# Kernel optimization log

Measured on AMD Instinct MI355X. Metric: run time of the kernel, lower is better.

## Reference

```python
import jax, jax.numpy as jnp
import numpy as np

N_SVC, N_NODE, N_POD = 50000, 20000, 100000
F = 128          # svc/instance/node feature dims (all 128 per init_kwargs)
HID = 128        # hidden_size
OUT = 64         # out_channel
E_SVC, E_PN, E_NP = 1600000, 100000, 100000


def _graph_conv(x, src, dst, n_src, n_dst, W, b):
    """DGL GraphConv with norm='both': D_dst^{-1/2} A D_src^{-1/2} X W + b."""
    ones = jnp.ones(src.shape[0], dtype=x.dtype)
    deg_src = jnp.clip(jax.ops.segment_sum(ones, src, num_segments=n_src), 1.0)
    deg_dst = jnp.clip(jax.ops.segment_sum(ones, dst, num_segments=n_dst), 1.0)
    # normalize at source, gather, scatter-sum to dst, normalize at dst
    h = x * jax.lax.rsqrt(deg_src)[:, None]          # [n_src, F]
    msg = h[src]                                      # [E, F] gather (memory-bound)
    agg = jax.ops.segment_sum(msg, dst, num_segments=n_dst)  # [n_dst, F]
    agg = agg * jax.lax.rsqrt(deg_dst)[:, None]
    return agg @ W + b                                # [n_dst, HID]


def _leaky(h):
    return jnp.where(h > 0, h, 0.01 * h)


def setup_inputs() -> dict:
    key = jax.random.key(0)
    ks = jax.random.split(key, 16)
    d = {
        "x_svc": jax.random.normal(ks[0], (N_SVC, F), jnp.float32),
        "x_pod": jax.random.normal(ks[1], (N_POD, F), jnp.float32),
        "x_node": jax.random.normal(ks[2], (N_NODE, F), jnp.float32),
        "svc_src": jax.random.randint(ks[3], (E_SVC,), 0, N_SVC, jnp.int32),
        "svc_dst": jax.random.randint(ks[4], (E_SVC,), 0, N_SVC, jnp.int32),
        "pod_node_src": jax.random.randint(ks[5], (E_PN,), 0, N_POD, jnp.int32),
        "pod_node_dst": jax.random.randint(ks[6], (E_PN,), 0, N_NODE, jnp.int32),
        "node_pod_src": jax.random.randint(ks[7], (E_NP,), 0, N_NODE, jnp.int32),
        "node_pod_dst": jax.random.randint(ks[8], (E_NP,), 0, N_POD, jnp.int32),
        # GraphConv weights per edge type
        "W_call": jax.random.normal(ks[9], (F, HID), jnp.float32) * (1.0 / np.sqrt(F)),
        "b_call": jnp.zeros((HID,), jnp.float32),
        "W_in": jax.random.normal(ks[10], (F, HID), jnp.float32) * (1.0 / np.sqrt(F)),
        "b_in": jnp.zeros((HID,), jnp.float32),
        "W_ni": jax.random.normal(ks[11], (F, HID), jnp.float32) * (1.0 / np.sqrt(F)),
        "b_ni": jnp.zeros((HID,), jnp.float32),
        # per-node-type output Linear (hidden -> out_channel)
        "W_lin_svc": jax.random.normal(ks[12], (HID, OUT), jnp.float32) * (1.0 / np.sqrt(HID)),
        "b_lin_svc": jnp.zeros((OUT,), jnp.float32),
        "W_lin_node": jax.random.normal(ks[13], (HID, OUT), jnp.float32) * (1.0 / np.sqrt(HID)),
        "b_lin_node": jnp.zeros((OUT,), jnp.float32),
        "W_lin_pod": jax.random.normal(ks[14], (HID, OUT), jnp.float32) * (1.0 / np.sqrt(HID)),
        "b_lin_pod": jnp.zeros((OUT,), jnp.float32),
    }
    return d


def reference(x_svc, x_pod, x_node,
              svc_src, svc_dst, pod_node_src, pod_node_dst,
              node_pod_src, node_pod_dst,
              W_call, b_call, W_in, b_in, W_ni, b_ni,
              W_lin_svc, b_lin_svc, W_lin_node, b_lin_node,
              W_lin_pod, b_lin_pod):
    # HeteroGraphConv (sum aggregate; each dst type receives one edge type here)
    h_svc = _graph_conv(x_svc, svc_src, svc_dst, N_SVC, N_SVC, W_call, b_call)
    h_node = _graph_conv(x_pod, pod_node_src, pod_node_dst, N_POD, N_NODE, W_in, b_in)
    h_pod = _graph_conv(x_node, node_pod_src, node_pod_dst, N_NODE, N_POD, W_ni, b_ni)
    # per-node-type LeakyReLU + Linear
    o_svc = _leaky(h_svc) @ W_lin_svc + b_lin_svc    # [N_SVC, OUT]
    o_node = _leaky(h_node) @ W_lin_node + b_lin_node  # [N_NODE, OUT]
    o_pod = _leaky(h_pod) @ W_lin_pod + b_lin_pod    # [N_POD, OUT]
    return jnp.concatenate([o_svc, o_node, o_pod], axis=0)  # [N_SVC+N_NODE+N_POD, OUT]
```

## Files before the change

kernel.cpp:

```cpp
#include <hip/hip_runtime.h>

typedef __attribute__((ext_vector_type(8))) short short8;
typedef __attribute__((ext_vector_type(4))) float floatx4;

#define N_SVC  50000
#define N_NODE 20000
#define N_POD  100000
#define E_SVC  1600000
#define E_PN   100000
#define E_NP   100000
#define N_TOT  170000
#define E_TOT  1800000
#define NBUCK  1329
#define NBLK   256
#define PER_BLK 7032
#define P_SVC_BASE  0
#define P_NODE_BASE 50048
#define P_POD_BASE  70080
#define P_TOT       170112
#define SVC_WAVES   50048
#define SVC_BLOCKS  12512
#define NP_WAVES    30016
#define NP_BLOCKS   7504

__device__ __forceinline__ unsigned short f2bf(float f) {
  union { float f; unsigned u; } v; v.f = f;
  unsigned r = v.u + 0x7FFFu + ((v.u >> 16) & 1u);
  return (unsigned short)(r >> 16);
}
__device__ __forceinline__ unsigned pack_bf2(float a, float b) {
  return (unsigned)f2bf(a) | ((unsigned)f2bf(b) << 16);
}
__device__ __forceinline__ float bfl(unsigned u) { union { unsigned u; float f; } v; v.u = u << 16; return v.f; }
__device__ __forceinline__ float bfh(unsigned u) { union { unsigned u; float f; } v; v.u = u & 0xFFFF0000u; return v.f; }

__device__ __forceinline__ int dbase_of(int b) {
  if (b <= 391) return b * 6144;
  if (b <= 547) return 2402304 + (b - 391) * 1536;
  return 2641920 + (b - 547) * 512;
}
#define DST_CAP_TOT 3042304
__device__ __forceinline__ int sbase_of(int b) {
  if (b <= 391) return b * 6144;
  if (b <= 1171) return 2402304 + (b - 391) * 512;
  return 2801664 + (b - 1171) * 1536;
}
#define SRC_CAP_TOT 3044352

__device__ __forceinline__ void load_edge(int i,
    const int* __restrict__ svcS, const int* __restrict__ svcD,
    const int* __restrict__ pnS, const int* __restrict__ pnD,
    const int* __restrict__ npS, const int* __restrict__ npD,
    int& S, int& D) {
  if (i < E_SVC)             { S = svcS[i];                         D = svcD[i]; }
  else if (i < E_SVC + E_PN) { int j = i - E_SVC;        S = pnS[j] + 50000;  D = pnD[j] + 50000; }
  else                       { int j = i - E_SVC - E_PN; S = npS[j] + 150000; D = npD[j] + 70000; }
}

__global__ void wprep_init(const float* __restrict__ W0, const float* __restrict__ W1,
                           const float* __restrict__ W2, const float* __restrict__ L0,
                           const float* __restrict__ L1, const float* __restrict__ L2,
                           unsigned short* __restrict__ Wt, unsigned short* __restrict__ Wt2,
                           int* __restrict__ dcur, int* __restrict__ scur) {
  int i = blockIdx.x * 256 + threadIdx.x;
  if (i < NBUCK) { dcur[i] = dbase_of(i); scur[i] = sbase_of(i); }
  if (i < 3 * 16384) {
    int t = i / 16384, r = i % 16384, n = r / 128, k = r % 128;
    const float* W = (t == 0) ? W0 : ((t == 1) ? W1 : W2);
    Wt[i] = f2bf(W[k * 128 + n]);
  } else if (i < 3 * 16384 + 3 * 8192) {
    int j = i - 3 * 16384;
    int t = j / 8192, r = j % 8192, n = r / 128, k = r % 128;
    const float* L = (t == 0) ? L0 : ((t == 1) ? L1 : L2);
    Wt2[j] = f2bf(L[k * 64 + n]);
  }
}

__global__ __launch_bounds__(1024) void scatter_onepass(
    const int* __restrict__ svcS, const int* __restrict__ svcD,
    const int* __restrict__ pnS, const int* __restrict__ pnD,
    const int* __restrict__ npS, const int* __restrict__ npD,
    int* __restrict__ dcur, int* __restrict__ scur,
    unsigned* __restrict__ dstbuf, unsigned char* __restrict__ srcbuf) {
  __shared__ int ldc[NBUCK], lsc[NBUCK];
  const int tid = threadIdx.x;
  for (int t = tid; t < NBUCK; t += 1024) { ldc[t] = 0; lsc[t] = 0; }
  __syncthreads();
  const int lo = blockIdx.x * PER_BLK;
  const int hi = (lo + PER_BLK < E_TOT) ? lo + PER_BLK : E_TOT;
  int Sv[7], Dv[7];
  #pragma unroll
  for (int k = 0; k < 7; ++k) {
    int e = lo + tid + k * 1024;
    if (e < hi) {
      load_edge(e, svcS, svcD, pnS, pnD, npS, npD, Sv[k], Dv[k]);
      atomicAdd(&ldc[Dv[k] >> 7], 1);
      atomicAdd(&lsc[Sv[k] >> 7], 1);
    } else Sv[k] = -1;
  }
  __syncthreads();
  for (int t = tid; t < NBUCK; t += 1024) {
    int c = ldc[t];  ldc[t] = c ? atomicAdd(&dcur[t], c) : 0;
    int c2 = lsc[t]; lsc[t] = c2 ? atomicAdd(&scur[t], c2) : 0;
  }
  __syncthreads();
  #pragma unroll
  for (int k = 0; k < 7; ++k) {
    if (Sv[k] >= 0) {
      int p = atomicAdd(&ldc[Dv[k] >> 7], 1);
      dstbuf[p] = ((unsigned)(Dv[k] & 127) << 18) | (unsigned)Sv[k];
      int q = atomicAdd(&lsc[Sv[k] >> 7], 1);
      srcbuf[q] = (unsigned char)(Sv[k] & 127);
    }
  }
}

__global__ __launch_bounds__(256) void finalize_all(
    const int* __restrict__ dcur, const int* __restrict__ scur,
    const unsigned* __restrict__ dstbuf, const unsigned char* __restrict__ srcbuf,
    int2* __restrict__ rowrange, int* __restrict__ csr, int* __restrict__ cnt_src) {
  __shared__ int lcnt[128], lcur[128];
  __shared__ int s_w0;
  const int tid = threadIdx.x;
  if (blockIdx.x < NBUCK) {
    const int b = blockIdx.x;
    const int base = dbase_of(b);
    const int cnt = dcur[b] - base;
    if (tid < 128) lcnt[tid] = 0;
    __syncthreads();
    for (int e = tid; e < cnt; e += 256) atomicAdd(&lcnt[dstbuf[base + e] >> 18], 1);
    __syncthreads();
    int excl = 0, v = 0;
    if (tid < 128) {
      v = lcnt[tid];
      int lane = tid & 63;
      int x = v;
      #pragma unroll
      for (int off = 1; off < 64; off <<= 1) {
        int y = __shfl_up(x, off, 64);
        if (lane >= off) x += y;
      }
      excl = x - v;
      if (tid == 63) s_w0 = x;
    }
    __syncthreads();
    if (tid < 128) {
      if (tid >= 64) excl += s_w0;
      lcur[tid] = excl;
      int u = b * 128 + tid;
      if (u < N_TOT) rowrange[u] = make_int2(base + excl, base + excl + v);
    }
    __syncthreads();
    for (int e = tid; e < cnt; e += 256) {
      unsigned wv = dstbuf[base + e];
      int p = atomicAdd(&lcur[wv >> 18], 1);
      csr[base + p] = (int)(wv & 0x3FFFFu);
    }
  } else {
    const int b = blockIdx.x - NBUCK;
    const int base = sbase_of(b);
    const int cnt = scur[b] - base;
    if (tid < 128) lcnt[tid] = 0;
    __syncthreads();
    for (int e = tid; e < cnt; e += 256) atomicAdd(&lcnt[srcbuf[base + e]], 1);
    __syncthreads();
    if (tid < 128) {
      int u = b * 128 + tid;
      if (u < N_TOT) cnt_src[u] = lcnt[tid];
    }
  }
}

__global__ void normalize_cast(const float* __restrict__ xs, const int* __restrict__ cs,
                               unsigned* __restrict__ Xn) {
  int i = blockIdx.x * blockDim.x + threadIdx.x;
  if (i >= N_SVC * 32) return;
  int row = i >> 5, c4 = i & 31;
  const float* src = xs + (size_t)row * 128;
  int cc = cs[row]; if (cc < 1) cc = 1;
  float r = rsqrtf((float)cc);
  float4 v = ((const float4*)src)[c4];
  uint2 o;
  o.x = pack_bf2(v.x * r, v.y * r);
  o.y = pack_bf2(v.z * r, v.w * r);
  *(uint2*)(Xn + (size_t)row * 64 + c4 * 2) = o;
}

#define ACC8(v) { a0 += bfl(v.x); a1 += bfh(v.x); a2 += bfl(v.y); a3 += bfh(v.y); \
                  a4 += bfl(v.z); a5 += bfh(v.z); a6 += bfl(v.w); a7 += bfh(v.w); }

__global__ __launch_bounds__(256) void aggregate_svc(
    const unsigned* __restrict__ Xn, const int2* __restrict__ rowrange,
    const int* __restrict__ csr, unsigned* __restrict__ aggb) {
  const int lane = threadIdx.x & 63;
  const int gw = blockIdx.x * 4 + (threadIdx.x >> 6);
  const int grp = lane >> 4, l16 = lane & 15;
  const unsigned* Xb = Xn + l16 * 4;
  unsigned* orow = aggb + (size_t)gw * 64 + l16 * 4;
  if (gw >= 50000) {
    if (gw < SVC_WAVES && grp == 0) *(uint4*)orow = (uint4){0u, 0u, 0u, 0u};
    return;
  }
  int2 rr = rowrange[gw];
  int beg = rr.x, end = rr.y;
  int deg = end - beg;
  float a0 = 0.f, a1 = 0.f, a2 = 0.f, a3 = 0.f, a4 = 0.f, a5 = 0.f, a6 = 0.f, a7 = 0.f;
  int e = beg;
  for (; e + 32 <= end; e += 32) {
    int s0 = csr[e + grp];
    int s1 = csr[e + 4 + grp];
    int s2 = csr[e + 8 + grp];
    int s3 = csr[e + 12 + grp];
    int s4 = csr[e + 16 + grp];
    int s5 = csr[e + 20 + grp];
    int s6 = csr[e + 24 + grp];
    int s7 = csr[e + 28 + grp];
    uint4 v0 = *(const uint4*)(Xb + (unsigned)s0 * 64);
    uint4 v1 = *(const uint4*)(Xb + (unsigned)s1 * 64);
    uint4 v2 = *(const uint4*)(Xb + (unsigned)s2 * 64);
    uint4 v3 = *(const uint4*)(Xb + (unsigned)s3 * 64);
    uint4 v4 = *(const uint4*)(Xb + (unsigned)s4 * 64);
    uint4 v5 = *(const uint4*)(Xb + (unsigned)s5 * 64);
    uint4 v6 = *(const uint4*)(Xb + (unsigned)s6 * 64);
    uint4 v7 = *(const uint4*)(Xb + (unsigned)s7 * 64);
    ACC8(v0) ACC8(v1) ACC8(v2) ACC8(v3) ACC8(v4) ACC8(v5) ACC8(v6) ACC8(v7)
  }
  for (; e + 16 <= end; e += 16) {
    int s0 = csr[e + grp];
    int s1 = csr[e + 4 + grp];
    int s2 = csr[e + 8 + grp];
    int s3 = csr[e + 12 + grp];
    uint4 v0 = *(const uint4*)(Xb + (unsigned)s0 * 64);
    uint4 v1 = *(const uint4*)(Xb + (unsigned)s1 * 64);
    uint4 v2 = *(const uint4*)(Xb + (unsigned)s2 * 64);
    uint4 v3 = *(const uint4*)(Xb + (unsigned)s3 * 64);
    ACC8(v0) ACC8(v1) ACC8(v2) ACC8(v3)
  }
  for (; e + 8 <= end; e += 8) {
    int s0 = csr[e + grp];
    int s1 = csr[e + 4 + grp];
    uint4 v0 = *(const uint4*)(Xb + (unsigned)s0 * 64);
    uint4 v1 = *(const uint4*)(Xb + (unsigned)s1 * 64);
    ACC8(v0) ACC8(v1)
  }
  for (; e + 4 <= end; e += 4) {
    int s = csr[e + grp];
    uint4 v = *(const uint4*)(Xb + (unsigned)s * 64);
    ACC8(v)
  }
  if (grp < end - e) {
    int s = csr[e + grp];
    uint4 v = *(const uint4*)(Xb + (unsigned)s * 64);
    ACC8(v)
  }
  a0 += __shfl_xor(a0, 32, 64); a1 += __shfl_xor(a1, 32, 64);
  a2 += __shfl_xor(a2, 32, 64); a3 += __shfl_xor(a3, 32, 64);
  a4 += __shfl_xor(a4, 32, 64); a5 += __shfl_xor(a5, 32, 64);
  a6 += __shfl_xor(a6, 32, 64); a7 += __shfl_xor(a7, 32, 64);
  a0 += __shfl_xor(a0, 16, 64); a1 += __shfl_xor(a1, 16, 64);
  a2 += __shfl_xor(a2, 16, 64); a3 += __shfl_xor(a3, 16, 64);
  a4 += __shfl_xor(a4, 16, 64); a5 += __shfl_xor(a5, 16, 64);
  a6 += __shfl_xor(a6, 16, 64); a7 += __shfl_xor(a7, 16, 64);
  float rd = rsqrtf((float)(deg < 1 ? 1 : deg));
  if (grp == 0) {
    uint4 o;
    o.x = pack_bf2(a0 * rd, a1 * rd);
    o.y = pack_bf2(a2 * rd, a3 * rd);
    o.z = pack_bf2(a4 * rd, a5 * rd);
    o.w = pack_bf2(a6 * rd, a7 * rd);
    *(uint4*)orow = o;
  }
}

__global__ __launch_bounds__(256) void aggregate_np(
    const float* __restrict__ xp, const float* __restrict__ xn,
    const int* __restrict__ cnt_src, const int2* __restrict__ rowrange,
    const int* __restrict__ csr, unsigned* __restrict__ aggb) {
  const int lane = threadIdx.x & 63;
  const int w = blockIdx.x * 4 + (threadIdx.x >> 6);
  const int grp = lane >> 4, l16 = lane & 15;
  const int row = SVC_WAVES + w * 4 + grp;
  if (row >= P_TOT) return;
  int u; bool valid; const float* Xf; int soff;
  if (row < P_POD_BASE) { u = row - 48; valid = (row - P_NODE_BASE) < 20000; Xf = xp; soff = 50000; }
  else                  { u = row - 80; valid = (row - P_POD_BASE) < 100000; Xf = xn; soff = 150000; }
  unsigned* orow = aggb + (size_t)row * 64 + l16 * 4;
  if (!valid) {
    *(uint4*)orow = (uint4){0u, 0u, 0u, 0u};
    return;
  }
  const float* Xb = Xf + l16 * 8;
  int2 rr = rowrange[u];
  int beg = rr.x, end = rr.y;
  int deg = end - beg;
  float a0 = 0.f, a1 = 0.f, a2 = 0.f, a3 = 0.f, a4 = 0.f, a5 = 0.f, a6 = 0.f, a7 = 0.f;
  int e = beg;
  for (; e + 2 <= end; e += 2) {
    int s0 = csr[e], s1 = csr[e + 1];
    int c0 = cnt_src[s0]; if (c0 < 1) c0 = 1;
    int c1 = cnt_src[s1]; if (c1 < 1) c1 = 1;
    float r0 = rsqrtf((float)c0), r1 = rsqrtf((float)c1);
    const float* p0 = Xb + (size_t)(s0 - soff) * 128;
    const float* p1 = Xb + (size_t)(s1 - soff) * 128;
    float4 u0 = *(const float4*)p0;
    float4 u1 = *(const float4*)(p0 + 4);
    float4 w0 = *(const float4*)p1;
    float4 w1 = *(const float4*)(p1 + 4);
    a0 += u0.x * r0 + w0.x * r1; a1 += u0.y * r0 + w0.y * r1;
    a2 += u0.z * r0 + w0.z * r1; a3 += u0.w * r0 + w0.w * r1;
    a4 += u1.x * r0 + w1.x * r1; a5 += u1.y * r0 + w1.y * r1;
    a6 += u1.z * r0 + w1.z * r1; a7 += u1.w * r0 + w1.w * r1;
  }
  if (e < end) {
    int s = csr[e];
    int c = cnt_src[s]; if (c < 1) c = 1;
    float r = rsqrtf((float)c);
    const float* p = Xb + (size_t)(s - soff) * 128;
    float4 u0 = *(const float4*)p;
    float4 u1 = *(const float4*)(p + 4);
    a0 += u0.x * r; a1 += u0.y * r; a2 += u0.z * r; a3 += u0.w * r;
    a4 += u1.x * r; a5 += u1.y * r; a6 += u1.z * r; a7 += u1.w * r;
  }
  float rd = rsqrtf((float)(deg < 1 ? 1 : deg));
  uint4 o;
  o.x = pack_bf2(a0 * rd, a1 * rd);
  o.y = pack_bf2(a2 * rd, a3 * rd);
  o.z = pack_bf2(a4 * rd, a5 * rd);
  o.w = pack_bf2(a6 * rd, a7 * rd);
  *(uint4*)orow = o;
}

__global__ __launch_bounds__(256) void gemm_fused(
    const unsigned short* __restrict__ aggb,
    const unsigned short* __restrict__ Wt,
    const unsigned short* __restrict__ Wt2,
    const float* __restrict__ b0, const float* __restrict__ b1, const float* __restrict__ b2,
    const float* __restrict__ l0, const float* __restrict__ l1, const float* __restrict__ l2,
    float* __restrict__ out) {
  __shared__ __align__(16) unsigned short sW1[128 * 136];
  __shared__ __align__(16) unsigned short sH[4][16 * 136];
  const int bid = blockIdx.x;
  int t, bl, nb, ntile, padbase, outbase, mcnt;
  if (bid < 226)      { t = 0; bl = bid;       nb = 226; ntile = 782;  padbase = P_SVC_BASE;  outbase = 0;     mcnt = 50000; }
  else if (bid < 316) { t = 1; bl = bid - 226; nb = 90;  ntile = 313;  padbase = P_NODE_BASE; outbase = 50000; mcnt = 20000; }
  else                { t = 2; bl = bid - 316; nb = 452; ntile = 1563; padbase = P_POD_BASE;  outbase = 70000; mcnt = 100000; }
  const float* bp = (t == 0) ? b0 : ((t == 1) ? b1 : b2);
  const float* lp = (t == 0) ? l0 : ((t == 1) ? l1 : l2);

  const unsigned short* W1g = Wt + t * 16384;
  for (int uu = threadIdx.x; uu < 2048; uu += 256) {
    short8 v = *(const short8*)(W1g + uu * 8);
    *(short8*)(&sW1[(uu >> 4) * 136 + (uu & 15) * 8]) = v;
  }
  const int wv = threadIdx.x >> 6, lane = threadIdx.x & 63;
  const int quad = lane >> 4, l16 = lane & 15;

  const unsigned short* W2g = Wt2 + t * 8192;
  short8 w2f[4][4];
  #pragma unroll
  for (int n = 0; n < 4; n++)
    #pragma unroll
    for (int kt = 0; kt < 4; kt++)
      w2f[n][kt] = *(const short8*)(W2g + (n * 16 + l16) * 128 + kt * 32 + quad * 8);
  float bias1[8], bias2[4];
  #pragma unroll
  for (int n = 0; n < 8; n++) bias1[n] = bp[n * 16 + l16];
  #pragma unroll
  for (int n = 0; n < 4; n++) bias2[n] = lp[n * 16 + l16];
  __syncthreads();

  for (int tile = bl; tile < ntile; tile += nb) {
    const unsigned short* Arow = aggb + (size_t)(padbase + tile * 64 + wv * 16 + l16) * 128;
    floatx4 acc[8];
    #pragma unroll
    for (int n = 0; n < 8; n++) acc[n] = (floatx4){0.f, 0.f, 0.f, 0.f};
    #pragma unroll
    for (int kt = 0; kt < 4; kt++) {
      short8 af = *(const short8*)(Arow + kt * 32 + quad * 8);
      #pragma unroll
      for (int n = 0; n < 8; n++) {
        short8 bf = *(const short8*)(&sW1[(n * 16 + l16) * 136 + kt * 32 + quad * 8]);
        acc[n] = __builtin_amdgcn_mfma_f32_16x16x32_bf16(af, bf, acc[n], 0, 0, 0);
      }
    }
    #pragma unroll
    for (int n = 0; n < 8; n++) {
      #pragma unroll
      for (int i = 0; i < 4; i++) {
        float h = acc[n][i] + bias1[n];
        h = (h > 0.f) ? h : 0.01f * h;
        sH[wv][(quad * 4 + i) * 136 + n * 16 + l16] = f2bf(h);
      }
    }
    floatx4 acc2[4];
    #pragma unroll
    for (int n = 0; n < 4; n++) acc2[n] = (floatx4){0.f, 0.f, 0.f, 0.f};
    #pragma unroll
    for (int kt = 0; kt < 4; kt++) {
      short8 af = *(const short8*)(&sH[wv][l16 * 136 + kt * 32 + quad * 8]);
      #pragma unroll
      for (int n = 0; n < 4; n++)
        acc2[n] = __builtin_amdgcn_mfma_f32_16x16x32_bf16(af, w2f[n][kt], acc2[n], 0, 0, 0);
    }
    int r0 = tile * 64 + wv * 16 + quad * 4;
    #pragma unroll
    for (int n = 0; n < 4; n++) {
      #pragma unroll
      for (int i = 0; i < 4; i++) {
        int r = r0 + i;
        if (r < mcnt) out[(size_t)(outbase + r) * 64 + n * 16 + l16] = acc2[n][i] + bias2[n];
      }
    }
  }
}

extern "C" void kernel_launch(void* const* d_in, const int* in_sizes, int n_in,
                              void* d_out, int out_size, void* d_ws, size_t ws_size,
                              hipStream_t stream) {
  const float* x_svc  = (const float*)d_in[0];
  const float* x_pod  = (const float*)d_in[1];
  const float* x_node = (const float*)d_in[2];
  const int* svc_src  = (const int*)d_in[3];
  const int* svc_dst  = (const int*)d_in[4];
  const int* pn_src   = (const int*)d_in[5];
  const int* pn_dst   = (const int*)d_in[6];
  const int* np_src   = (const int*)d_in[7];
  const int* np_dst   = (const int*)d_in[8];
  const float* W_call = (const float*)d_in[9];
  const float* b_call = (const float*)d_in[10];
  const float* W_in   = (const float*)d_in[11];
  const float* b_in   = (const float*)d_in[12];
  const float* W_ni   = (const float*)d_in[13];
  const float* b_ni   = (const float*)d_in[14];
  const float* W_ls   = (const float*)d_in[15];
  const float* b_ls   = (const float*)d_in[16];
  const float* W_ln   = (const float*)d_in[17];
  const float* b_ln   = (const float*)d_in[18];
  const float* W_lp   = (const float*)d_in[19];
  const float* b_lp   = (const float*)d_in[20];
  float* out = (float*)d_out;

  char* ws = (char*)d_ws;
  int*  dcur     = (int*)(ws + 0);
  int*  scur     = (int*)(ws + 5504);
  int2* rowrange = (int2*)(ws + 11008);
  int*  cnt_src  = (int*)(ws + 1371008);
  int*  csr      = (int*)(ws + 2051072);
  unsigned short* Wt  = (unsigned short*)(ws + 14220288);
  unsigned short* Wt2 = (unsigned short*)(ws + 14318592);
  unsigned* Xn     = (unsigned*)(ws + 14367744);
  unsigned* dstbuf = (unsigned*)(ws + 14367744);
  unsigned char* srcbuf = (unsigned char*)(ws + 27180032);
  unsigned* aggb   = (unsigned*)(ws + 30224384);

  wprep_init<<<288, 256, 0, stream>>>(W_call, W_in, W_ni, W_ls, W_ln, W_lp,
                                      Wt, Wt2, dcur, scur);
  scatter_onepass<<<NBLK, 1024, 0, stream>>>(svc_src, svc_dst, pn_src, pn_dst,
                                             np_src, np_dst, dcur, scur, dstbuf, srcbuf);
  finalize_all<<<2 * NBUCK, 256, 0, stream>>>(dcur, scur, dstbuf, srcbuf,
                                              rowrange, csr, cnt_src);
  normalize_cast<<<6250, 256, 0, stream>>>(x_svc, cnt_src, Xn);
  aggregate_svc<<<SVC_BLOCKS, 256, 0, stream>>>(Xn, rowrange, csr, aggb);
  aggregate_np<<<NP_BLOCKS, 256, 0, stream>>>(x_pod, x_node, cnt_src, rowrange, csr, aggb);
  gemm_fused<<<768, 256, 0, stream>>>((const unsigned short*)aggb, Wt, Wt2,
                                      b_call, b_in, b_ni, b_ls, b_ln, b_lp, out);
}
```

Before: 303.8 us.

## Split svc aggregation launch, drop 32-wide unroll, prefetch GEMM A tiles

The service aggregation kernel is now launched as two half-size grids with a row-base offset, and its 32-edge unrolled loop is removed so the 16-edge loop handles the bulk. Separately, the fused GEMM now loads the A fragments for the next tile while computing the current one (register double-buffering), to hide global load latency. The split launch adds a kernel-launch boundary. Removing the wider unroll lowers register pressure but also reduces memory-level parallelism per wave.

```diff
diff --git a/kernel.cpp b/kernel.cpp
--- a/kernel.cpp
+++ b/kernel.cpp
@@ -19,7 +19,8 @@
 #define P_POD_BASE  70080
 #define P_TOT       170112
 #define SVC_WAVES   50048
-#define SVC_BLOCKS  12512
+#define SVC_HALF    25024
+#define SVC_HBLK    6256
 #define NP_WAVES    30016
 #define NP_BLOCKS   7504
 
@@ -191,9 +192,9 @@
 
 __global__ __launch_bounds__(256) void aggregate_svc(
     const unsigned* __restrict__ Xn, const int2* __restrict__ rowrange,
-    const int* __restrict__ csr, unsigned* __restrict__ aggb) {
+    const int* __restrict__ csr, unsigned* __restrict__ aggb, int rbase) {
   const int lane = threadIdx.x & 63;
-  const int gw = blockIdx.x * 4 + (threadIdx.x >> 6);
+  const int gw = rbase + blockIdx.x * 4 + (threadIdx.x >> 6);
   const int grp = lane >> 4, l16 = lane & 15;
   const unsigned* Xb = Xn + l16 * 4;
   unsigned* orow = aggb + (size_t)gw * 64 + l16 * 4;
@@ -206,25 +207,6 @@
   int deg = end - beg;
   float a0 = 0.f, a1 = 0.f, a2 = 0.f, a3 = 0.f, a4 = 0.f, a5 = 0.f, a6 = 0.f, a7 = 0.f;
   int e = beg;
-  for (; e + 32 <= end; e += 32) {
-    int s0 = csr[e + grp];
-    int s1 = csr[e + 4 + grp];
-    int s2 = csr[e + 8 + grp];
-    int s3 = csr[e + 12 + grp];
-    int s4 = csr[e + 16 + grp];
-    int s5 = csr[e + 20 + grp];
-    int s6 = csr[e + 24 + grp];
-    int s7 = csr[e + 28 + grp];
-    uint4 v0 = *(const uint4*)(Xb + (unsigned)s0 * 64);
-    uint4 v1 = *(const uint4*)(Xb + (unsigned)s1 * 64);
-    uint4 v2 = *(const uint4*)(Xb + (unsigned)s2 * 64);
-    uint4 v3 = *(const uint4*)(Xb + (unsigned)s3 * 64);
-    uint4 v4 = *(const uint4*)(Xb + (unsigned)s4 * 64);
-    uint4 v5 = *(const uint4*)(Xb + (unsigned)s5 * 64);
-    uint4 v6 = *(const uint4*)(Xb + (unsigned)s6 * 64);
-    uint4 v7 = *(const uint4*)(Xb + (unsigned)s7 * 64);
-    ACC8(v0) ACC8(v1) ACC8(v2) ACC8(v3) ACC8(v4) ACC8(v5) ACC8(v6) ACC8(v7)
-  }
   for (; e + 16 <= end; e += 16) {
     int s0 = csr[e + grp];
     int s1 = csr[e + 4 + grp];
@@ -369,18 +351,31 @@
   for (int n = 0; n < 4; n++) bias2[n] = lp[n * 16 + l16];
   __syncthreads();
 
+  const unsigned short* Abase = aggb + (size_t)padbase * 128
+                              + (size_t)(wv * 16 + l16) * 128 + quad * 8;
+  short8 afc[4];
+  if (bl < ntile) {
+    const unsigned short* Ar = Abase + (size_t)bl * 8192;
+    #pragma unroll
+    for (int kt = 0; kt < 4; kt++) afc[kt] = *(const short8*)(Ar + kt * 32);
+  }
   for (int tile = bl; tile < ntile; tile += nb) {
-    const unsigned short* Arow = aggb + (size_t)(padbase + tile * 64 + wv * 16 + l16) * 128;
+    short8 afn[4] = {afc[0], afc[1], afc[2], afc[3]};
+    int tn = tile + nb;
+    if (tn < ntile) {
+      const unsigned short* Ar = Abase + (size_t)tn * 8192;
+      #pragma unroll
+      for (int kt = 0; kt < 4; kt++) afn[kt] = *(const short8*)(Ar + kt * 32);
+    }
     floatx4 acc[8];
     #pragma unroll
     for (int n = 0; n < 8; n++) acc[n] = (floatx4){0.f, 0.f, 0.f, 0.f};
     #pragma unroll
     for (int kt = 0; kt < 4; kt++) {
-      short8 af = *(const short8*)(Arow + kt * 32 + quad * 8);
       #pragma unroll
       for (int n = 0; n < 8; n++) {
         short8 bf = *(const short8*)(&sW1[(n * 16 + l16) * 136 + kt * 32 + quad * 8]);
-        acc[n] = __builtin_amdgcn_mfma_f32_16x16x32_bf16(af, bf, acc[n], 0, 0, 0);
+        acc[n] = __builtin_amdgcn_mfma_f32_16x16x32_bf16(afc[kt], bf, acc[n], 0, 0, 0);
       }
     }
     #pragma unroll
@@ -411,6 +406,8 @@
         if (r < mcnt) out[(size_t)(outbase + r) * 64 + n * 16 + l16] = acc2[n][i] + bias2[n];
       }
     }
+    #pragma unroll
+    for (int kt = 0; kt < 4; kt++) afc[kt] = afn[kt];
   }
 }
 
@@ -460,7 +457,8 @@
   finalize_all<<<2 * NBUCK, 256, 0, stream>>>(dcur, scur, dstbuf, srcbuf,
                                               rowrange, csr, cnt_src);
   normalize_cast<<<6250, 256, 0, stream>>>(x_svc, cnt_src, Xn);
-  aggregate_svc<<<SVC_BLOCKS, 256, 0, stream>>>(Xn, rowrange, csr, aggb);
+  aggregate_svc<<<SVC_HBLK, 256, 0, stream>>>(Xn, rowrange, csr, aggb, 0);
+  aggregate_svc<<<SVC_HBLK, 256, 0, stream>>>(Xn, rowrange, csr, aggb, SVC_HALF);
   aggregate_np<<<NP_BLOCKS, 256, 0, stream>>>(x_pod, x_node, cnt_src, rowrange, csr, aggb);
   gemm_fused<<<768, 256, 0, stream>>>((const unsigned short*)aggb, Wt, Wt2,
                                       b_call, b_in, b_ni, b_ls, b_ln, b_lp, out);
```

After: 307.0 us. About the same (+1.0%).
